# Kernel optimization log

Hardware: AMD Instinct MI355X
Metric: run time of the kernel (lower is better)

## Reference

```python
import jax, jax.numpy as jnp
import numpy as np

LN_EPS = 1e-5

def layer_norm(x, gamma, beta):
    mu = jnp.mean(x, axis=-1, keepdims=True)
    var = jnp.mean(jnp.square(x - mu), axis=-1, keepdims=True)
    return (x - mu) * jax.lax.rsqrt(var + LN_EPS) * gamma + beta

def setup_inputs() -> dict:
    key = jax.random.key(0)
    ks = jax.random.split(key, 10)
    B, C, N = 8, 256, 4096
    s = 1.0 / np.sqrt(C)
    inp = {
        "x": jax.random.normal(ks[0], (B, C, N), dtype=jnp.float32),
        "W_qkv": jax.random.uniform(ks[1], (C, C), jnp.float32, -s, s),            # Linear(dim, dim, bias=False)
        "W_mlp": jax.random.uniform(ks[2], (2 * C, 2 * C), jnp.float32, -0.5 * s, 0.5 * s),
        "b_mlp": jax.random.uniform(ks[3], (2 * C,), jnp.float32, -0.5 * s, 0.5 * s),
        "g1": jnp.ones((4 * C,), jnp.float32),
        "beta1": jnp.zeros((4 * C,), jnp.float32),
        "W_res": jax.random.uniform(ks[4], (C, 4 * C), jnp.float32, -0.25 * s, 0.25 * s),  # Linear(4*dim, dim, bias=False)
        "g2": jnp.ones((C,), jnp.float32),
        "beta2": jnp.zeros((C,), jnp.float32),
    }
    return inp

def reference(x, W_qkv, W_mlp, b_mlp, g1, beta1, W_res, g2, beta2):
    # x: (B, C, N) channels-first -> (B, N, C)
    NITER = 2  # niter_heads
    x = jnp.swapaxes(x, 1, 2)
    x = x @ W_qkv.T                                   # shared_qkv, (B, N, C)
    v = jax.lax.stop_gradient(x)                      # x.clone().detach()
    for _ in range(NITER):
        # first_context = x^T @ v : (B, C, C)
        ctx = jnp.einsum('bnc,bnd->bcd', x, v)
        out = jax.nn.softmax(x, axis=-1) @ ctx        # (B, N, C)
        cat1 = jnp.concatenate([out, v], axis=-1)     # (B, N, 2C)
        mlp = jax.nn.relu(cat1 @ W_mlp.T + b_mlp)     # (B, N, 2C)
        cat2 = jnp.concatenate([cat1, mlp], axis=-1)  # (B, N, 4C)
        # dropout layers are identity in eval mode
        v = layer_norm(cat2, g1, beta1) @ W_res.T + x # residual_mlp + skip
        v = layer_norm(x + v, g2, beta2)
    return jnp.swapaxes(v, 1, 2)                      # back to (B, C, N)
```

## Files before the change

### kernel.cpp

```cpp
#include <hip/hip_runtime.h>
#include <cstdint>
#include <cstddef>


using u16 = unsigned short;
using short8 = __attribute__((ext_vector_type(8))) short;
using bf16x8 = __attribute__((ext_vector_type(8))) __bf16;
using f32x4  = __attribute__((ext_vector_type(4))) float;
using i32x4  = __attribute__((ext_vector_type(4))) int;
using u16x4  = __attribute__((ext_vector_type(4))) u16;
using u16x8  = __attribute__((ext_vector_type(8))) u16;

__device__ __forceinline__ float b2f(u16 u) {
    union { unsigned u32; float f; } c; c.u32 = ((unsigned)u) << 16; return c.f;
}
__device__ __forceinline__ u16 f2b(float f) {
    union { float f; unsigned u; } c; c.f = f;
    unsigned r = c.u + 0x7FFFu + ((c.u >> 16) & 1u);
    return (u16)(r >> 16);
}
__device__ __forceinline__ void cvt(u16 a,  u16& o)   { o = a; }
__device__ __forceinline__ void cvt(float a, u16& o)  { o = f2b(a); }
__device__ __forceinline__ void cvt(float a, float& o){ o = a; }
__device__ __forceinline__ void cvt(u16 a,  float& o) { o = b2f(a); }

__device__ __forceinline__ void glds16(const u16* g, short* l) {
    __builtin_amdgcn_global_load_lds(
        (const __attribute__((address_space(1))) void*)g,
        (__attribute__((address_space(3))) void*)l, 16, 0, 0);
}

template<int MODE, int TRF>
__global__ __launch_bounds__(512)
void gemm_bt(const u16* __restrict__ A, const u16* __restrict__ A2,
             const u16* __restrict__ A3,
             int lda, int lda2, int lda3, int kSplit,
             const u16* __restrict__ B, int ldb, long strA, long strB,
             int statStride, int kChunk, int nKsplit,
             float* __restrict__ outF, u16* __restrict__ outB,
             long sOF, long sOB, int ldo,
             const u16* __restrict__ Xres,
             const float* __restrict__ bias,
             const float2* __restrict__ stats,
             const float* __restrict__ g, const float* __restrict__ be)
{
    __shared__ short lsA[2][128 * 64];
    __shared__ short lsB[2][128 * 64];

    const int bz    = blockIdx.z;
    const int batch = bz / nKsplit;
    const int ks    = bz - batch * nKsplit;
    const u16* Ab = A + (size_t)batch * strA;
    const u16* Bb = B + (size_t)batch * strB;
    const int colBase = blockIdx.x * 128;
    const int rowBase = blockIdx.y * 128;
    const int k0 = ks * kChunk;
    const int k1 = k0 + kChunk;

    const int t    = threadIdx.x;
    const int sRow = t >> 3;
    const int sKl  = (t & 7) << 3;
    const int sKg  = (((t & 7) ^ (sRow & 7)) << 3);

    const int lane = t & 63;
    const int w    = t >> 6;
    const int wr   = (w >> 1) * 32;
    const int wc   = (w & 1) * 64;
    const int mrow = lane & 15;
    const int q    = lane >> 4;

    float2 st0 = {0.f, 0.f}, st1 = {0.f, 0.f};
    if (TRF == 1) {
        const int sb = batch * statStride + rowBase;
        st0 = stats[sb + sRow];
        st1 = stats[sb + sRow + 64];
    }

    auto aPtr = [&](int rloc, int kn) -> const u16* {
        const int arow = rowBase + rloc + sRow;
        if (TRF == 2) {
            if (kn < 256)      return A  + (size_t)arow * lda  + kn + sKg;
            else if (kn < 512) return A2 + (size_t)arow * lda2 + (kn - 256) + sKg;
            else               return A3 + (size_t)arow * lda3 + (kn - 512) + sKg;
        } else if (TRF == 3) {
            if (kn < kSplit)   return Ab + (size_t)arow * lda + kn + sKg;
            return A2 + (size_t)arow * lda2 + (kn - kSplit) + sKg;
        }
        return Ab + (size_t)arow * lda + kn + sKg;
    };
    auto rawA = [&](int rloc, int kn) -> i32x4 {
        const int arow = rowBase + rloc + sRow;
        return *(const i32x4*)(Ab + (size_t)arow * lda + kn + sKg);
    };
    auto xf = [&](i32x4 raw, float2 st) -> i32x4 {
        short8 h = __builtin_bit_cast(short8, raw);
        short8 o;
#pragma unroll
        for (int i = 0; i < 8; i++) {
            float v = b2f((u16)h[i]);
            v = __expf(v - st.x) * st.y;
            o[i] = (short)f2b(v);
        }
        return __builtin_bit_cast(i32x4, o);
    };

    const f32x4 fzero = {0.f, 0.f, 0.f, 0.f};
    f32x4 acc[2][4];
#pragma unroll
    for (int i = 0; i < 2; i++)
#pragma unroll
        for (int j = 0; j < 4; j++) acc[i][j] = fzero;

    const u16* pB0 = Bb + (size_t)(colBase + sRow) * ldb + sKg;
    const u16* pB1 = pB0 + (size_t)64 * ldb;
    const u16* pA0 = nullptr; const u16* pA1 = nullptr;
    if (TRF == 0) {
        pA0 = Ab + (size_t)(rowBase + sRow) * lda + sKg;
        pA1 = pA0 + (size_t)64 * lda;
    }

    const int rsw = mrow & 7;
    const int kc0 = (((0 * 4 + q) ^ rsw) << 3);
    const int kc1 = (((1 * 4 + q) ^ rsw) << 3);

    auto stageB = [&](int buf, int kk) {
        glds16(pB0 + kk, &lsB[buf][w * 512]);
        glds16(pB1 + kk, &lsB[buf][4096 + w * 512]);
    };
    auto stageA = [&](int buf, int kk) {
        if (TRF == 0) {
            glds16(pA0 + kk, &lsA[buf][w * 512]);
            glds16(pA1 + kk, &lsA[buf][4096 + w * 512]);
        } else {
            glds16(aPtr(0,  kk), &lsA[buf][w * 512]);
            glds16(aPtr(64, kk), &lsA[buf][4096 + w * 512]);
        }
    };

    i32x4 ra0, ra1;
    if (TRF == 1) {
        ra0 = rawA(0, k0); ra1 = rawA(64, k0);
        *(i32x4*)&lsA[0][sRow * 64 + sKl]        = xf(ra0, st0);
        *(i32x4*)&lsA[0][(sRow + 64) * 64 + sKl] = xf(ra1, st1);
        stageB(0, k0);
    } else {
        stageA(0, k0);
        stageB(0, k0);
    }
    __syncthreads();

    int cur = 0;
    for (int kk = k0; kk < k1; kk += 64) {
        const int kn = kk + 64;
        const bool more = kn < k1;
        if (more) {
            if (TRF == 1) {
                ra0 = rawA(0, kn); ra1 = rawA(64, kn);
                stageB(cur ^ 1, kn);
            } else {
                stageA(cur ^ 1, kn);
                stageB(cur ^ 1, kn);
            }
        }
#pragma unroll
        for (int h = 0; h < 2; h++) {
            const int kc = h ? kc1 : kc0;
            bf16x8 af[2], bfr[4];
#pragma unroll
            for (int mi = 0; mi < 2; mi++)
                af[mi] = __builtin_bit_cast(bf16x8,
                    *(const short8*)&lsA[cur][(wr + mi * 16 + mrow) * 64 + kc]);
#pragma unroll
            for (int ni = 0; ni < 4; ni++)
                bfr[ni] = __builtin_bit_cast(bf16x8,
                    *(const short8*)&lsB[cur][(wc + ni * 16 + mrow) * 64 + kc]);
#pragma unroll
            for (int mi = 0; mi < 2; mi++)
#pragma unroll
                for (int ni = 0; ni < 4; ni++)
                    acc[mi][ni] = __builtin_amdgcn_mfma_f32_16x16x32_bf16(
                        af[mi], bfr[ni], acc[mi][ni], 0, 0, 0);
        }
        if (more) {
            if (TRF == 1) {
                *(i32x4*)&lsA[cur ^ 1][sRow * 64 + sKl]        = xf(ra0, st0);
                *(i32x4*)&lsA[cur ^ 1][(sRow + 64) * 64 + sKl] = xf(ra1, st1);
            }
            __syncthreads();
            cur ^= 1;
        }
    }

#pragma unroll
    for (int mi = 0; mi < 2; mi++) {
#pragma unroll
        for (int ni = 0; ni < 4; ni++) {
            const int col = colBase + wc + ni * 16 + mrow;
#pragma unroll
            for (int r = 0; r < 4; r++) {
                const int row = rowBase + wr + mi * 16 + q * 4 + r;
                float v = acc[mi][ni][r];
                if (MODE == 0) {
                    outB[(size_t)batch * sOB + (size_t)row * ldo + col] = f2b(v);
                } else if (MODE == 1) {
                    outF[((size_t)batch * nKsplit + ks) * sOF
                         + (size_t)row * ldo + col] = v;
                } else if (MODE == 3) {
                    v += bias[col];
                    v = v > 0.f ? v : 0.f;
                    outB[(size_t)row * ldo + col] = f2b(v);
                } else if (MODE == 4) {
                    const float2 ln = stats[row];
                    v = ln.y * (v - ln.x * g[col]) + be[col]
                        + 2.f * b2f(Xres[(size_t)row * 256 + col]);
                    outB[(size_t)row * ldo + col] = f2b(v);
                }
            }
        }
    }
}

template<typename TIN, typename TOUT>
__global__ __launch_bounds__(256)
void transpose_k(const TIN* __restrict__ in, TOUT* __restrict__ out,
                 int R, int Cc, long sIn, long sOut)
{
    __shared__ TOUT tile[32][33];
    const int b = blockIdx.z;
    const TIN* ib = in + (size_t)b * sIn;
    TOUT* ob = out + (size_t)b * sOut;
    const int c0 = blockIdx.x * 32, r0 = blockIdx.y * 32;
    const int tx = threadIdx.x & 31, ty = threadIdx.x >> 5;
#pragma unroll
    for (int i = 0; i < 32; i += 8)
        cvt(ib[(size_t)(r0 + ty + i) * Cc + c0 + tx], tile[ty + i][tx]);
    __syncthreads();
#pragma unroll
    for (int i = 0; i < 32; i += 8)
        ob[(size_t)(c0 + ty + i) * R + r0 + tx] = tile[tx][ty + i];
}

__global__ __launch_bounds__(256)
void smstats_k(const u16* __restrict__ Xb, float2* __restrict__ st)
{
    const int wave = threadIdx.x >> 6, lane = threadIdx.x & 63;
    const size_t row = (size_t)blockIdx.x * 4 + wave;
    const u16x4 xb = *(const u16x4*)(Xb + row * 256 + lane * 4);
    const float x0 = b2f(xb.x), x1 = b2f(xb.y), x2 = b2f(xb.z), x3 = b2f(xb.w);
    float m = fmaxf(fmaxf(x0, x1), fmaxf(x2, x3));
    for (int o = 32; o > 0; o >>= 1) m = fmaxf(m, __shfl_xor(m, o));
    float s = __expf(x0 - m) + __expf(x1 - m) + __expf(x2 - m) + __expf(x3 - m);
    for (int o = 32; o > 0; o >>= 1) s += __shfl_xor(s, o);
    if (lane == 0) st[row] = make_float2(m, 1.f / s);
}

__global__ __launch_bounds__(256)
void stats1024_k(const u16* __restrict__ OUT, const u16* __restrict__ V,
                 const u16* __restrict__ MLPo, float2* __restrict__ st)
{
    const int wave = threadIdx.x >> 6, lane = threadIdx.x & 63;
    const size_t row = (size_t)blockIdx.x * 4 + wave;
    const int c = lane * 16;
    const u16* src;
    if (c < 256)       src = OUT  + row * 256 + c;
    else if (c < 512)  src = V    + row * 256 + (c - 256);
    else               src = MLPo + row * 512 + (c - 512);
    short8 r0 = *(const short8*)(src);
    short8 r1 = *(const short8*)(src + 8);
    float s = 0.f, s2 = 0.f;
#pragma unroll
    for (int i = 0; i < 8; i++) {
        const float a = b2f((u16)r0[i]), b = b2f((u16)r1[i]);
        s += a + b; s2 += a * a + b * b;
    }
    for (int o = 32; o > 0; o >>= 1) { s += __shfl_xor(s, o); s2 += __shfl_xor(s2, o); }
    const float mean = s * (1.f / 1024.f);
    const float var  = s2 * (1.f / 1024.f) - mean * mean;
    if (lane == 0) st[row] = make_float2(mean, rsqrtf(var + 1e-5f));
}

template<typename OUTT, bool WRITE_VB>
__global__ __launch_bounds__(256)
void ln256t_k(const u16* __restrict__ Tb, const float* __restrict__ g,
              const float* __restrict__ be, u16* __restrict__ Vb,
              OUTT* __restrict__ outT)
{
    constexpr int STRIDE = (sizeof(OUTT) == 2) ? 266 : 261;
    __shared__ OUTT tile[32 * STRIDE];
    const int wid = threadIdx.x >> 6, lane = threadIdx.x & 63;
    const int bx = blockIdx.x;
    const size_t r0 = (size_t)bx * 32;
    const int b  = bx >> 7;
    const int n0 = (bx & 127) * 32;

#pragma unroll
    for (int j = 0; j < 8; j++) {
        const int lr = wid * 8 + j;
        const size_t row = r0 + lr;
        const u16x4 tb = *(const u16x4*)(Tb + row * 256 + lane * 4);
        const float x0 = b2f(tb.x), x1 = b2f(tb.y), x2 = b2f(tb.z), x3 = b2f(tb.w);
        float s  = x0 + x1 + x2 + x3;
        float s2 = x0 * x0 + x1 * x1 + x2 * x2 + x3 * x3;
        for (int o = 32; o > 0; o >>= 1) { s += __shfl_xor(s, o); s2 += __shfl_xor(s2, o); }
        const float mean = s * (1.f / 256.f);
        const float var  = s2 * (1.f / 256.f) - mean * mean;
        const float rstd = rsqrtf(var + 1e-5f);
        const int c = lane * 4;
        float4 ov = { (x0 - mean) * rstd * g[c + 0] + be[c + 0],
                      (x1 - mean) * rstd * g[c + 1] + be[c + 1],
                      (x2 - mean) * rstd * g[c + 2] + be[c + 2],
                      (x3 - mean) * rstd * g[c + 3] + be[c + 3] };
        if (WRITE_VB) {
            u16x4 vb = { f2b(ov.x), f2b(ov.y), f2b(ov.z), f2b(ov.w) };
            *(u16x4*)(Vb + row * 256 + c) = vb;
        }
        OUTT* tl = &tile[lr * STRIDE + c];
        cvt(ov.x, tl[0]); cvt(ov.y, tl[1]); cvt(ov.z, tl[2]); cvt(ov.w, tl[3]);
    }
    __syncthreads();

    const int c = threadIdx.x;
    OUTT* dst = outT + ((size_t)b * 256 + c) * 4096 + n0;
    if (sizeof(OUTT) == 2) {
#pragma unroll
        for (int k = 0; k < 4; k++) {
            u16x8 v;
#pragma unroll
            for (int i = 0; i < 8; i++) v[i] = *(const u16*)&tile[(k * 8 + i) * STRIDE + c];
            *(u16x8*)((u16*)dst + k * 8) = v;
        }
    } else {
#pragma unroll
        for (int k = 0; k < 8; k++) {
            float4 v;
            v.x = *(const float*)&tile[(k * 4 + 0) * STRIDE + c];
            v.y = *(const float*)&tile[(k * 4 + 1) * STRIDE + c];
            v.z = *(const float*)&tile[(k * 4 + 2) * STRIDE + c];
            v.w = *(const float*)&tile[(k * 4 + 3) * STRIDE + c];
            *(float4*)((float*)dst + k * 4) = v;
        }
    }
}

__global__ __launch_bounds__(256)
void ctxreduce_k(const float* __restrict__ ctxp, u16* __restrict__ ctxb)
{
    const int i = blockIdx.x * 256 + threadIdx.x;
    const int batch  = i >> 14;
    const int within = i & 16383;
    const float4* src = (const float4*)ctxp + (size_t)batch * 16 * 16384 + within;
    float4 s = {0.f, 0.f, 0.f, 0.f};
#pragma unroll
    for (int ks = 0; ks < 16; ks++) {
        const float4 v = src[(size_t)ks * 16384];
        s.x += v.x; s.y += v.y; s.z += v.z; s.w += v.w;
    }
    u16x4 o = { f2b(s.x), f2b(s.y), f2b(s.z), f2b(s.w) };
    ((u16x4*)ctxb)[i] = o;
}

__global__ __launch_bounds__(256)
void wconv_k(const float* __restrict__ Wq, const float* __restrict__ Wm,
             u16* __restrict__ oq, u16* __restrict__ om)
{
    const int i = blockIdx.x * 256 + threadIdx.x;
    const float* src; u16* dst; int j;
    if (i < 16384) { src = Wq; dst = oq; j = i; }
    else           { src = Wm; dst = om; j = i - 16384; }
    const float4 v = ((const float4*)src)[j];
    u16x4 o = { f2b(v.x), f2b(v.y), f2b(v.z), f2b(v.w) };
    ((u16x4*)dst)[j] = o;
}

__global__ __launch_bounds__(256)
void wresprep_k(const float* __restrict__ Wres, const float* __restrict__ g1,
                const float* __restrict__ be1, u16* __restrict__ Wr_b,
                float* __restrict__ sg, float* __restrict__ br)
{
    const int wv = threadIdx.x >> 6, lane = threadIdx.x & 63;
    const int row = blockIdx.x * 4 + wv;
    const float* src = Wres + (size_t)row * 1024;
    float s = 0.f, b = 0.f;
#pragma unroll
    for (int j = 0; j < 4; j++) {
        const int c = j * 256 + lane * 4;
        const float4 w  = *(const float4*)(src + c);
        const float4 gg = *(const float4*)(g1 + c);
        const float4 bb = *(const float4*)(be1 + c);
        const float4 wg = { w.x * gg.x, w.y * gg.y, w.z * gg.z, w.w * gg.w };
        u16x4 o = { f2b(wg.x), f2b(wg.y), f2b(wg.z), f2b(wg.w) };
        *(u16x4*)(Wr_b + (size_t)row * 1024 + c) = o;
        s += wg.x + wg.y + wg.z + wg.w;
        b += w.x * bb.x + w.y * bb.y + w.z * bb.z + w.w * bb.w;
    }
    for (int o = 32; o > 0; o >>= 1) { s += __shfl_xor(s, o); b += __shfl_xor(b, o); }
    if (lane == 0) { sg[row] = s; br[row] = b; }
}

extern "C" void kernel_launch(void* const* d_in, const int* in_sizes, int n_in,
                              void* d_out, int out_size, void* d_ws, size_t ws_size,
                              hipStream_t stream)
{
    (void)in_sizes; (void)n_in; (void)out_size; (void)ws_size;
    const float* x    = (const float*)d_in[0];
    const float* Wqkv = (const float*)d_in[1];
    const float* Wmlp = (const float*)d_in[2];
    const float* bmlp = (const float*)d_in[3];
    const float* g1   = (const float*)d_in[4];
    const float* be1  = (const float*)d_in[5];
    const float* Wres = (const float*)d_in[6];
    const float* g2   = (const float*)d_in[7];
    const float* be2  = (const float*)d_in[8];

    char* ws = (char*)d_ws;
    u16*    Xb   = (u16*)ws;    ws += (size_t)16777216;
    u16*    XT   = (u16*)ws;    ws += (size_t)16777216;
    u16*    Vb   = (u16*)ws;    ws += (size_t)16777216;
    u16*    VT2  = (u16*)ws;    ws += (size_t)16777216;
    u16*    OUT  = (u16*)ws;    ws += (size_t)16777216;
    u16*    MLPo = (u16*)ws;    ws += (size_t)33554432;
    u16*    Tb   = (u16*)ws;    ws += (size_t)16777216;
    float*  ctxp = (float*)ws;  ws += (size_t)33554432;
    u16*    ctxb = (u16*)ws;    ws += (size_t)1048576;
    float2* smst = (float2*)ws; ws += (size_t)262144;
    float2* lnst = (float2*)ws; ws += (size_t)262144;
    u16*    Wq_b = (u16*)ws;    ws += (size_t)131072;
    u16*    Wm_b = (u16*)ws;    ws += (size_t)524288;
    u16*    Wr_b = (u16*)ws;    ws += (size_t)524288;
    float*  sg   = (float*)ws;  ws += (size_t)1024;
    float*  br   = (float*)ws;  ws += (size_t)1024;
    u16*    xt   = MLPo;

    wconv_k<<<dim3(320), 256, 0, stream>>>(Wqkv, Wmlp, Wq_b, Wm_b);
    wresprep_k<<<dim3(64), 256, 0, stream>>>(Wres, g1, be1, Wr_b, sg, br);

    transpose_k<float, u16><<<dim3(128, 8, 8), 256, 0, stream>>>(
        x, xt, 256, 4096, 256L * 4096, 4096L * 256);

    gemm_bt<0, 0><<<dim3(2, 256, 1), 512, 0, stream>>>(
        xt, nullptr, nullptr, 256, 0, 0, 0, Wq_b, 256, 0, 0, 0, 256, 1,
        nullptr, Xb, 0, 0, 256, nullptr, nullptr, nullptr, nullptr, nullptr);

    smstats_k<<<dim3(8192), 256, 0, stream>>>(Xb, smst);

    transpose_k<u16, u16><<<dim3(8, 128, 8), 256, 0, stream>>>(
        Xb, XT, 4096, 256, 4096L * 256, 256L * 4096);

    const u16* VTcur = XT;
    const u16* Vcur  = Xb;

    for (int it = 0; it < 2; ++it) {
        gemm_bt<1, 0><<<dim3(2, 2, 128), 512, 0, stream>>>(
            VTcur, nullptr, nullptr, 4096, 0, 0, 0, XT, 4096,
            1048576, 1048576, 0, 256, 16,
            ctxp, nullptr, 65536, 0, 256, nullptr, nullptr, nullptr, nullptr, nullptr);
        ctxreduce_k<<<dim3(512), 256, 0, stream>>>(ctxp, ctxb);

        gemm_bt<0, 1><<<dim3(2, 32, 8), 512, 0, stream>>>(
            Xb, nullptr, nullptr, 256, 0, 0, 0, ctxb, 256,
            1048576, 65536, 4096, 256, 1,
            nullptr, OUT, 0, 1048576, 256, nullptr, nullptr, smst, nullptr, nullptr);

        gemm_bt<3, 3><<<dim3(4, 256, 1), 512, 0, stream>>>(
            OUT, Vcur, nullptr, 256, 256, 0, 256, Wm_b, 512, 0, 0, 0, 512, 1,
            nullptr, MLPo, 0, 0, 512, nullptr, bmlp, nullptr, nullptr, nullptr);

        stats1024_k<<<dim3(8192), 256, 0, stream>>>(OUT, Vcur, MLPo, lnst);

        gemm_bt<4, 2><<<dim3(2, 256, 1), 512, 0, stream>>>(
            OUT, Vcur, MLPo, 256, 256, 512, 0, Wr_b, 1024, 0, 0, 0, 1024, 1,
            nullptr, Tb, 0, 0, 256, Xb, nullptr, lnst, sg, br);

        if (it == 0) {
            ln256t_k<u16, true><<<dim3(1024), 256, 0, stream>>>(
                Tb, g2, be2, Vb, VT2);
            VTcur = VT2;
            Vcur  = Vb;
        } else {
            ln256t_k<float, false><<<dim3(1024), 256, 0, stream>>>(
                Tb, g2, be2, nullptr, (float*)d_out);
        }
    }
}
```

Measured before the change: 366.9 us.

## Triple-buffer A tiles with explicit vmcnt waits and MFMA priority in GEMM

In the non-transforming GEMM path, the single-sync double-buffered loop becomes a deeper pipeline. A tiles are triple-buffered and B tiles double-buffered, with direct global-to-LDS loads issued up to three tiles ahead. Manual s_waitcnt vmcnt counts and raw s_barriers replace __syncthreads, and s_setprio raises wave priority during the MFMA burst. This aims to hide global load latency and the barrier stalls between K-steps, at the cost of more shared memory per block (possibly lower occupancy) and reliance on hand-counted outstanding loads.

```diff
diff --git a/kernel.cpp b/kernel.cpp
--- a/kernel.cpp
+++ b/kernel.cpp
@@ -44,8 +44,8 @@
              const float2* __restrict__ stats,
              const float* __restrict__ g, const float* __restrict__ be)
 {
-    __shared__ short lsA[2][128 * 64];
-    __shared__ short lsB[2][128 * 64];
+    __shared__ short lsA[3 * 8192];
+    __shared__ short lsB[2 * 8192];
 
     const int bz    = blockIdx.z;
     const int batch = bz / nKsplit;
@@ -123,45 +123,17 @@
     const int kc0 = (((0 * 4 + q) ^ rsw) << 3);
     const int kc1 = (((1 * 4 + q) ^ rsw) << 3);
 
-    auto stageB = [&](int buf, int kk) {
-        glds16(pB0 + kk, &lsB[buf][w * 512]);
-        glds16(pB1 + kk, &lsB[buf][4096 + w * 512]);
-    };
-    auto stageA = [&](int buf, int kk) {
-        if (TRF == 0) {
-            glds16(pA0 + kk, &lsA[buf][w * 512]);
-            glds16(pA1 + kk, &lsA[buf][4096 + w * 512]);
-        } else {
-            glds16(aPtr(0,  kk), &lsA[buf][w * 512]);
-            glds16(aPtr(64, kk), &lsA[buf][4096 + w * 512]);
-        }
-    };
-
-    i32x4 ra0, ra1;
-    if (TRF == 1) {
-        ra0 = rawA(0, k0); ra1 = rawA(64, k0);
-        *(i32x4*)&lsA[0][sRow * 64 + sKl]        = xf(ra0, st0);
-        *(i32x4*)&lsA[0][(sRow + 64) * 64 + sKl] = xf(ra1, st1);
-        stageB(0, k0);
-    } else {
-        stageA(0, k0);
-        stageB(0, k0);
-    }
-    __syncthreads();
-
-    int cur = 0;
-    for (int kk = k0; kk < k1; kk += 64) {
-        const int kn = kk + 64;
-        const bool more = kn < k1;
-        if (more) {
-            if (TRF == 1) {
-                ra0 = rawA(0, kn); ra1 = rawA(64, kn);
-                stageB(cur ^ 1, kn);
-            } else {
-                stageA(cur ^ 1, kn);
-                stageB(cur ^ 1, kn);
-            }
-        }
+    auto stageA2 = [&](int buf, int kk) {
+        short* d0 = &lsA[buf * 8192 + w * 512];
+        short* d1 = &lsA[buf * 8192 + 4096 + w * 512];
+        if (TRF == 0) { glds16(pA0 + kk, d0); glds16(pA1 + kk, d1); }
+        else          { glds16(aPtr(0, kk), d0); glds16(aPtr(64, kk), d1); }
+    };
+    auto stageB2 = [&](int buf, int kk) {
+        glds16(pB0 + kk, &lsB[buf * 8192 + w * 512]);
+        glds16(pB1 + kk, &lsB[buf * 8192 + 4096 + w * 512]);
+    };
+    auto compute = [&](int bufA, int bufB) {
 #pragma unroll
         for (int h = 0; h < 2; h++) {
             const int kc = h ? kc1 : kc0;
@@ -169,25 +141,67 @@
 #pragma unroll
             for (int mi = 0; mi < 2; mi++)
                 af[mi] = __builtin_bit_cast(bf16x8,
-                    *(const short8*)&lsA[cur][(wr + mi * 16 + mrow) * 64 + kc]);
+                    *(const short8*)&lsA[bufA * 8192 + (wr + mi * 16 + mrow) * 64 + kc]);
 #pragma unroll
             for (int ni = 0; ni < 4; ni++)
                 bfr[ni] = __builtin_bit_cast(bf16x8,
-                    *(const short8*)&lsB[cur][(wc + ni * 16 + mrow) * 64 + kc]);
+                    *(const short8*)&lsB[bufB * 8192 + (wc + ni * 16 + mrow) * 64 + kc]);
+            __builtin_amdgcn_s_setprio(1);
 #pragma unroll
             for (int mi = 0; mi < 2; mi++)
 #pragma unroll
                 for (int ni = 0; ni < 4; ni++)
                     acc[mi][ni] = __builtin_amdgcn_mfma_f32_16x16x32_bf16(
                         af[mi], bfr[ni], acc[mi][ni], 0, 0, 0);
-        }
-        if (more) {
-            if (TRF == 1) {
-                *(i32x4*)&lsA[cur ^ 1][sRow * 64 + sKl]        = xf(ra0, st0);
-                *(i32x4*)&lsA[cur ^ 1][(sRow + 64) * 64 + sKl] = xf(ra1, st1);
+            __builtin_amdgcn_s_setprio(0);
+        }
+    };
+
+    if (TRF == 1) {
+        i32x4 ra0, ra1;
+        ra0 = rawA(0, k0); ra1 = rawA(64, k0);
+        *(i32x4*)&lsA[sRow * 64 + sKl]        = xf(ra0, st0);
+        *(i32x4*)&lsA[(sRow + 64) * 64 + sKl] = xf(ra1, st1);
+        stageB2(0, k0);
+        __syncthreads();
+        int cur = 0;
+        for (int kk = k0; kk < k1; kk += 64) {
+            const int kn = kk + 64;
+            const bool more = kn < k1;
+            if (more) {
+                ra0 = rawA(0, kn); ra1 = rawA(64, kn);
+                stageB2(cur ^ 1, kn);
             }
-            __syncthreads();
-            cur ^= 1;
+            compute(cur, cur);
+            if (more) {
+                *(i32x4*)&lsA[(cur ^ 1) * 8192 + sRow * 64 + sKl]        = xf(ra0, st0);
+                *(i32x4*)&lsA[(cur ^ 1) * 8192 + (sRow + 64) * 64 + sKl] = xf(ra1, st1);
+                __syncthreads();
+                cur ^= 1;
+            }
+        }
+    } else {
+        const int nt = kChunk >> 6;
+        stageB2(0, k0);
+        stageA2(0, k0);
+        stageB2(1, k0 + 64);
+        stageA2(1, k0 + 64);
+        stageA2(2, k0 + 128);
+        int bufA = 0, bufB = 0;
+        for (int tt = 0; tt < nt; ++tt) {
+            if (tt + 2 < nt)       asm volatile("s_waitcnt vmcnt(6)" ::: "memory");
+            else if (tt + 2 == nt) asm volatile("s_waitcnt vmcnt(4)" ::: "memory");
+            else                   asm volatile("s_waitcnt vmcnt(0)" ::: "memory");
+            __builtin_amdgcn_s_barrier();
+            __builtin_amdgcn_sched_barrier(0);
+            compute(bufA, bufB);
+            __builtin_amdgcn_sched_barrier(0);
+            __builtin_amdgcn_s_barrier();
+            const int kk = k0 + tt * 64;
+            if (tt + 2 < nt) stageB2(bufB, kk + 128);
+            if (tt + 3 < nt) stageA2(bufA, kk + 192);
+            bufA = (bufA == 2) ? 0 : bufA + 1;
+            bufB ^= 1;
         }
     }
 
```

Measured after the change: 371.8 us. No clear change (+1.3%).
